# Kernel optimization log

Hardware: AMD Instinct MI355X
Metric: run time of the kernel (lower is better)

The kernel has to match this reference:

```python
import jax, jax.numpy as jnp
from jax import lax
import numpy as np

COMMITMENT = 0.25

def conv(x, w, b, stride, pad):
    # x: NCHW, w: OIHW
    y = lax.conv_general_dilated(x, w, (stride, stride), [(pad, pad), (pad, pad)],
                                 dimension_numbers=('NCHW', 'OIHW', 'NCHW'))
    return y + b[None, :, None, None]

def up2(x):
    # PyTorch nn.Upsample(scale_factor=2, mode='bilinear', align_corners=False)
    b, c, h, w = x.shape
    return jax.image.resize(x, (b, c, 2 * h, 2 * w), method='bilinear')

def vq(z, emb):
    # z: (B, D, H, W); emb: (K, D)
    zc = jnp.transpose(z, (0, 2, 3, 1))          # b h w d
    sh = zc.shape
    flat = zc.reshape(-1, sh[-1])                # (N, D)
    dist = (jnp.sum(flat ** 2, axis=1, keepdims=True)
            + jnp.sum(emb ** 2, axis=1)
            - 2.0 * flat @ emb.T)                # (N, K)
    idx = jnp.argmin(dist, axis=1)               # (N,)
    q = emb[idx].reshape(sh)                     # gather == one-hot @ emb
    e_loss = (lax.stop_gradient(q) - zc) ** 2
    q_loss = (q - lax.stop_gradient(zc)) ** 2
    loss = q_loss + COMMITMENT * e_loss          # (b, h, w, d)
    q_st = zc + lax.stop_gradient(q - zc)        # straight-through
    return jnp.transpose(q_st, (0, 3, 1, 2)), loss

def setup_inputs() -> dict:
    key = jax.random.key(0)
    ks = jax.random.split(key, 32)
    S, K, D, IC = 64, 1024, 64, 3
    def w(k, shape, scale=0.05):
        return jax.random.normal(k, shape, jnp.float32) * scale
    z = lambda n: jnp.zeros((n,), jnp.float32)
    return {
        'x': jax.random.normal(ks[0], (8, IC, 256, 256), jnp.float32),
        'ew1': w(ks[1], (S, IC, 3, 3)),        'eb1': z(S),
        'ew2': w(ks[2], (2 * S, S, 3, 3)),     'eb2': z(2 * S),
        'ew3': w(ks[3], (4 * S, 2 * S, 3, 3)), 'eb3': z(4 * S),
        'ew4': w(ks[4], (8 * S, 4 * S, 3, 3)), 'eb4': z(8 * S),
        'pqw': w(ks[5], (D, 8 * S, 1, 1)),     'pqb': z(D),
        'emb': jax.random.uniform(ks[6], (K, D), jnp.float32, -1.0 / K, 1.0 / K),
        'poqw': w(ks[7], (8 * S, D, 1, 1)),    'poqb': z(8 * S),
        'dw1': w(ks[8], (8 * S, 8 * S, 3, 3)), 'db1': z(8 * S),
        'dw2': w(ks[9], (4 * S, 8 * S, 3, 3)), 'db2': z(4 * S),
        'dw3': w(ks[10], (2 * S, 4 * S, 3, 3)),'db3': z(2 * S),
        'dw4': w(ks[11], (S, 2 * S, 3, 3)),    'db4': z(S),
        'ow': w(ks[12], (IC, S, 3, 3)),        'ob': z(IC),
    }

def reference(x, ew1, eb1, ew2, eb2, ew3, eb3, ew4, eb4, pqw, pqb, emb,
              poqw, poqb, dw1, db1, dw2, db2, dw3, db3, dw4, db4, ow, ob):
    silu = jax.nn.silu
    h = silu(conv(x, ew1, eb1, 1, 1))
    h = silu(conv(h, ew2, eb2, 2, 1))
    h = silu(conv(h, ew3, eb3, 2, 1))
    h = conv(h, ew4, eb4, 2, 1)
    zq = conv(h, pqw, pqb, 1, 0)
    q, loss = vq(zq, emb)
    d = conv(q, poqw, poqb, 1, 0)
    d = up2(silu(conv(d, dw1, db1, 1, 1)))
    d = up2(silu(conv(d, dw2, db2, 1, 1)))
    d = up2(silu(conv(d, dw3, db3, 1, 1)))
    d = conv(d, dw4, db4, 1, 1)
    out = jax.nn.sigmoid(conv(d, ow, ob, 1, 1))
    return out, loss
```

## Files before the change

### kernel.cpp

```cpp
#include <hip/hip_runtime.h>
#include <hip/hip_bf16.h>
#include <math.h>

typedef __hip_bfloat16 bf16;
typedef __attribute__((ext_vector_type(8))) short short8;
typedef __attribute__((ext_vector_type(4))) float f32x4;

static __device__ __forceinline__ float bf2f(unsigned short u) {
  return __uint_as_float(((unsigned int)u) << 16);
}
static __device__ __forceinline__ unsigned short f2bf_bits(float f) {
  unsigned int x = __float_as_uint(f);
  x += 0x7fffu + ((x >> 16) & 1u);
  return (unsigned short)(x >> 16);
}
static __device__ __forceinline__ void sto_bf(bf16* p, float v) {
  *reinterpret_cast<unsigned short*>(p) = f2bf_bits(v);
}
struct F4 { float a, b, c, d; };
static __device__ __forceinline__ F4 ld4bf(const bf16* p) {
  uint2 u = *reinterpret_cast<const uint2*>(p);
  return { bf2f((unsigned short)(u.x & 0xffffu)), bf2f((unsigned short)(u.x >> 16)),
           bf2f((unsigned short)(u.y & 0xffffu)), bf2f((unsigned short)(u.y >> 16)) };
}

static __device__ __forceinline__ void g2l16(const void* g, void* l) {
  __builtin_amdgcn_global_load_lds(
      (const __attribute__((address_space(1))) unsigned int*)g,
      (__attribute__((address_space(3))) unsigned int*)l, 16, 0, 0);
}

__global__ __launch_bounds__(256) void wx_toc(const float* __restrict__ src,
                                              bf16* __restrict__ hi, bf16* __restrict__ lo,
                                              int OC, int IC, int T) {
  int total = T * OC * IC;
  int i = blockIdx.x * 256 + threadIdx.x;
  if (i >= total) return;
  int tap = i / (OC * IC); int r = i - tap * OC * IC;
  int oc = r / IC; int ic = r - oc * IC;
  float v = src[(oc * IC + ic) * T + tap];
  float h = bf2f(f2bf_bits(v));
  sto_bf(hi + i, h);
  if (lo) sto_bf(lo + i, v - h);
}
__global__ __launch_bounds__(256) void wx_tico(const float* __restrict__ src,
                                               float* __restrict__ dst,
                                               int OC, int IC, int T) {
  int total = T * OC * IC;
  int i = blockIdx.x * 256 + threadIdx.x;
  if (i >= total) return;
  int tap = i / (IC * OC); int r = i - tap * IC * OC;
  int ic = r / OC; int oc = r - ic * OC;
  dst[i] = src[(oc * IC + ic) * T + tap];
}

__global__ __launch_bounds__(256) void bzero_knl(bf16* __restrict__ buf, int N, int Hp, int Wp, int C) {
  long per = 2 * Wp + 2 * Hp - 4;
  long total = (long)N * per * C;
  long t = (long)blockIdx.x * 256 + threadIdx.x;
  if (t >= total) return;
  int c = (int)(t % C); long q = t / C;
  int pos = (int)(q % per); int n = (int)(q / per);
  int y, x;
  if (pos < Wp) { y = 0; x = pos; }
  else if (pos < 2 * Wp) { y = Hp - 1; x = pos - Wp; }
  else { int r = pos - 2 * Wp; y = 1 + (r >> 1); x = (r & 1) ? Wp - 1 : 0; }
  *reinterpret_cast<unsigned short*>(&buf[(((long)n * Hp + y) * Wp + x) * C + c]) = 0;
}

template <bool SPLIT, int BM, bool TAP9>
__global__ __launch_bounds__(256) void conv_mfma(
    const bf16* __restrict__ inhi, const bf16* __restrict__ inlo,
    int IHp, int IWp, int IC, int kcLog, int stride,
    const bf16* __restrict__ whi, const bf16* __restrict__ wlo,
    const float* __restrict__ bias, int OC, int OH, int OW,
    int omode, int opad, int OHp, int OWp, int silu,
    void* __restrict__ outp, bf16* __restrict__ outlo)
{
  constexpr int NB = SPLIT ? 2 : 1;
  constexpr int AIW = BM / 32;
  constexpr int MREP = 2;
  constexpr int NREP = (BM == 128) ? 4 : 2;
  __shared__ uint4 ldsA[2][NB][BM * 8];
  __shared__ uint4 ldsB[2][NB][64 * 8];

  const int tid = threadIdx.x;
  const int lane = tid & 63;
  const int wv = tid >> 6;
  const int pixBase = blockIdx.x * BM;
  const int ocBase = blockIdx.y * 64;
  const int OHW = OH * OW;

  int aoff[AIW], asl[AIW];
#pragma unroll
  for (int j = 0; j < AIW; ++j) {
    int I = wv * AIW + j;
    int m = I * 8 + (lane >> 3);
    int icoff = ((lane & 7) ^ (m & 7)) * 8;
    int p = pixBase + m;
    int n = p / OHW; int r = p - n * OHW;
    int oy = r / OW; int ox = r - oy * OW;
    aoff[j] = ((n * IHp + oy * stride) * IWp + ox * stride) * IC + icoff;
    asl[j] = I * 64 + lane;
  }
  int boff[2], bsl[2];
#pragma unroll
  for (int j = 0; j < 2; ++j) {
    int I = wv * 2 + j;
    int ocr = I * 8 + (lane >> 3);
    int icoff = ((lane & 7) ^ (ocr & 7)) * 8;
    boff[j] = (ocBase + ocr) * IC + icoff;
    bsl[j] = I * 64 + lane;
  }

  const int kcMask = (1 << kcLog) - 1;
  const int steps = (TAP9 ? 9 : 1) << kcLog;

  auto stage = [&](int buf, int s) {
    int tap = s >> kcLog;
    int k0 = (s & kcMask) << 6;
    int ta = 0;
    if (TAP9) { int ky = tap / 3, kx = tap - ky * 3; ta = (ky * IWp + kx) * IC; }
    int ga = ta + k0;
#pragma unroll
    for (int j = 0; j < AIW; ++j) {
      g2l16(inhi + aoff[j] + ga, &ldsA[buf][0][asl[j]]);
      if constexpr (SPLIT) g2l16(inlo + aoff[j] + ga, &ldsA[buf][1][asl[j]]);
    }
    int gb = tap * OC * IC + k0;
#pragma unroll
    for (int j = 0; j < 2; ++j) {
      g2l16(whi + boff[j] + gb, &ldsB[buf][0][bsl[j]]);
      if constexpr (SPLIT) g2l16(wlo + boff[j] + gb, &ldsB[buf][1][bsl[j]]);
    }
  };

  const int wrow = (BM == 128) ? wv * 32 : (wv >> 1) * 32;
  const int wcol = (BM == 128) ? 0 : (wv & 1) * 32;

  f32x4 acc[MREP][NREP];
#pragma unroll
  for (int i = 0; i < MREP; ++i)
#pragma unroll
    for (int j = 0; j < NREP; ++j) { acc[i][j][0] = 0.f; acc[i][j][1] = 0.f; acc[i][j][2] = 0.f; acc[i][j][3] = 0.f; }

  stage(0, 0);
  __syncthreads();
  int cur = 0;
  for (int s = 0; s < steps; ++s) {
    if (s + 1 < steps) stage(cur ^ 1, s + 1);
#pragma unroll
    for (int kk = 0; kk < 2; ++kk) {
      int kb = kk * 4 + (lane >> 4);
      short8 af[NB][MREP], bfr[NB][NREP];
#pragma unroll
      for (int mr = 0; mr < MREP; ++mr) {
        int row = wrow + mr * 16 + (lane & 15);
        int slot = row * 8 + (kb ^ (row & 7));
        af[0][mr] = *(const short8*)&ldsA[cur][0][slot];
        if constexpr (SPLIT) af[1][mr] = *(const short8*)&ldsA[cur][1][slot];
      }
#pragma unroll
      for (int nr = 0; nr < NREP; ++nr) {
        int ocr = wcol + nr * 16 + (lane & 15);
        int slot = ocr * 8 + (kb ^ (ocr & 7));
        bfr[0][nr] = *(const short8*)&ldsB[cur][0][slot];
        if constexpr (SPLIT) bfr[1][nr] = *(const short8*)&ldsB[cur][1][slot];
      }
#pragma unroll
      for (int mr = 0; mr < MREP; ++mr)
#pragma unroll
        for (int nr = 0; nr < NREP; ++nr) {
          acc[mr][nr] = __builtin_amdgcn_mfma_f32_16x16x32_bf16(af[0][mr], bfr[0][nr], acc[mr][nr], 0, 0, 0);
          if constexpr (SPLIT) {
            acc[mr][nr] = __builtin_amdgcn_mfma_f32_16x16x32_bf16(af[1][mr], bfr[0][nr], acc[mr][nr], 0, 0, 0);
            acc[mr][nr] = __builtin_amdgcn_mfma_f32_16x16x32_bf16(af[0][mr], bfr[1][nr], acc[mr][nr], 0, 0, 0);
          }
        }
    }
    __syncthreads();
    cur ^= 1;
  }

#pragma unroll
  for (int mr = 0; mr < MREP; ++mr) {
#pragma unroll
    for (int nr = 0; nr < NREP; ++nr) {
      int col = ocBase + wcol + nr * 16 + (lane & 15);
      float bv = bias[col];
#pragma unroll
      for (int r = 0; r < 4; ++r) {
        int row = wrow + mr * 16 + (lane >> 4) * 4 + r;
        float v = acc[mr][nr][r] + bv;
        if (silu) v = v / (1.f + expf(-v));
        int p = pixBase + row;
        if (omode == 0) {
          ((float*)outp)[p * OC + col] = v;
        } else {
          int n = p / OHW; int rr = p - n * OHW;
          int oy = rr / OW; int ox = rr - oy * OW;
          int ob = ((n * OHp + oy + opad) * OWp + ox + opad) * OC + col;
          float h = bf2f(f2bf_bits(v));
          sto_bf((bf16*)outp + ob, h);
          if (omode == 2) sto_bf(outlo + ob, v - h);
        }
      }
    }
  }
}

__global__ __launch_bounds__(256) void e1_knl(const float* __restrict__ x,
                                              const float* __restrict__ w,
                                              const float* __restrict__ bias,
                                              bf16* __restrict__ ahi, bf16* __restrict__ alo) {
  int gw = (blockIdx.x << 2) | (threadIdx.x >> 6);
  int lane = threadIdx.x & 63;
  int ox0 = (gw & 63) << 2;
  int oy = (gw >> 6) & 255;
  int n = gw >> 14;

  float wr[27];
#pragma unroll
  for (int j = 0; j < 27; ++j) wr[j] = w[j * 64 + lane];

  float bv = bias[lane];
  float acc[4] = {bv, bv, bv, bv};

#pragma unroll
  for (int ky = 0; ky < 3; ++ky) {
    int iy = oy - 1 + ky;
    if ((unsigned)iy < 256u) {
#pragma unroll
      for (int ic = 0; ic < 3; ++ic) {
        const float* xr = x + ((n * 3 + ic) * 256 + iy) * 256;
        float xv[6];
#pragma unroll
        for (int j = 0; j < 6; ++j) {
          int ix = ox0 - 1 + j;
          xv[j] = ((unsigned)ix < 256u) ? xr[ix] : 0.f;
        }
#pragma unroll
        for (int kx = 0; kx < 3; ++kx) {
          float wv = wr[(ky * 3 + kx) * 3 + ic];
#pragma unroll
          for (int p = 0; p < 4; ++p) acc[p] = fmaf(xv[p + kx], wv, acc[p]);
        }
      }
    }
  }
#pragma unroll
  for (int p = 0; p < 4; ++p) {
    float v = acc[p] / (1.f + __expf(-acc[p]));
    long ob = (((long)n * 258 + oy + 1) * 258 + (ox0 + p + 1)) * 64 + lane;
    float h = bf2f(f2bf_bits(v));
    sto_bf(ahi + ob, h);
    sto_bf(alo + ob, v - h);
  }
}

__global__ __launch_bounds__(256) void up2_knl(const bf16* __restrict__ in, bf16* __restrict__ out,
                                               int N, int H, int W, int C) {
  int C4 = C >> 2;
  int OW = 2 * W, OH = 2 * H;
  long total = (long)N * OH * OW * C4;
  long tid = (long)blockIdx.x * 256 + threadIdx.x;
  if (tid >= total) return;
  int c4 = (int)(tid % C4); long t = tid / C4;
  int ox = (int)(t % OW); t /= OW;
  int oy = (int)(t % OH); int n = (int)(t / OH);
  float sy = 0.5f * oy - 0.25f, sx = 0.5f * ox - 0.25f;
  int y0 = (int)floorf(sy); float fy = sy - (float)y0;
  int x0 = (int)floorf(sx); float fx = sx - (float)x0;
  int y0c = y0 < 0 ? 0 : y0; int y1c = (y0 + 1 > H - 1) ? (H - 1) : (y0 + 1);
  int x0c = x0 < 0 ? 0 : x0; int x1c = (x0 + 1 > W - 1) ? (W - 1) : (x0 + 1);
  const bf16* base = in + (long)n * H * W * C + c4 * 4;
  F4 t00 = ld4bf(base + ((long)y0c * W + x0c) * C);
  F4 t01 = ld4bf(base + ((long)y0c * W + x1c) * C);
  F4 t10 = ld4bf(base + ((long)y1c * W + x0c) * C);
  F4 t11 = ld4bf(base + ((long)y1c * W + x1c) * C);
  float w00 = (1.f - fy) * (1.f - fx), w01 = (1.f - fy) * fx;
  float w10 = fy * (1.f - fx), w11 = fy * fx;
  union { unsigned short us[4]; uint2 u; } pk;
  pk.us[0] = f2bf_bits(w00 * t00.a + w01 * t01.a + w10 * t10.a + w11 * t11.a);
  pk.us[1] = f2bf_bits(w00 * t00.b + w01 * t01.b + w10 * t10.b + w11 * t11.b);
  pk.us[2] = f2bf_bits(w00 * t00.c + w01 * t01.c + w10 * t10.c + w11 * t11.c);
  pk.us[3] = f2bf_bits(w00 * t00.d + w01 * t01.d + w10 * t10.d + w11 * t11.d);
  *reinterpret_cast<uint2*>(out + (((long)n * (OH + 2) + oy + 1) * (OW + 2) + ox + 1) * C + c4 * 4) = pk.u;
}

__global__ __launch_bounds__(256) void zsplit_knl(const float* __restrict__ src,
                                                  bf16* __restrict__ hi, bf16* __restrict__ lo, int n) {
  int i = blockIdx.x * 256 + threadIdx.x;
  if (i >= n) return;
  float v = src[i];
  float h = bf2f(f2bf_bits(v));
  sto_bf(hi + i, h);
  sto_bf(lo + i, v - h);
}
__global__ __launch_bounds__(256) void nbias_knl(const float* __restrict__ emb, float* __restrict__ nb) {
  int k = blockIdx.x * 256 + threadIdx.x;
  if (k >= 1024) return;
  float s = 0.f;
#pragma unroll
  for (int d = 0; d < 64; ++d) { float e = emb[k * 64 + d]; s = fmaf(e, e, s); }
  nb[k] = -0.5f * s;
}
__global__ __launch_bounds__(256) void vq2_knl(const float* __restrict__ S,
                                               const float* __restrict__ zq,
                                               const float* __restrict__ emb,
                                               bf16* __restrict__ q, float* __restrict__ loss) {
  __shared__ float sd[256];
  __shared__ int si[256];
  int row = blockIdx.x;
  int tid = threadIdx.x;
  const float* Sr = S + (long)row * 1024;
  float best = -3.4e38f; int bi = 0;
#pragma unroll
  for (int j = 0; j < 4; ++j) {
    int k = tid + j * 256;
    float v = Sr[k];
    if (v > best) { best = v; bi = k; }
  }
  sd[tid] = best; si[tid] = bi;
  __syncthreads();
  for (int s = 128; s > 0; s >>= 1) {
    if (tid < s) {
      float od = sd[tid + s]; int oi = si[tid + s];
      if (od > sd[tid] || (od == sd[tid] && oi < si[tid])) { sd[tid] = od; si[tid] = oi; }
    }
    __syncthreads();
  }
  int idx = si[0];
  if (tid < 64) {
    float e = emb[(long)idx * 64 + tid];
    float zv = zq[(long)row * 64 + tid];
    float d = e - zv;
    sto_bf(q + (long)row * 64 + tid, e);
    loss[(long)row * 64 + tid] = 1.25f * d * d;
  }
}

__global__ __launch_bounds__(256) void outc_knl(const bf16* __restrict__ in,
                                                const float* __restrict__ w,
                                                const float* __restrict__ bias,
                                                float* __restrict__ out) {
  int pix = blockIdx.x * 256 + threadIdx.x;
  int x = pix & 255;
  int y = (pix >> 8) & 255;
  int n = pix >> 16;
  float a0 = bias[0], a1 = bias[1], a2 = bias[2];
#pragma unroll
  for (int ky = 0; ky < 3; ++ky) {
#pragma unroll
    for (int kx = 0; kx < 3; ++kx) {
      const bf16* ip = in + (((long)(n * 258 + y + ky)) * 258 + (x + kx)) * 64;
      const int t = ky * 3 + kx;
#pragma unroll
      for (int g = 0; g < 8; ++g) {
        short8 v = *reinterpret_cast<const short8*>(ip + g * 8);
#pragma unroll
        for (int j = 0; j < 8; ++j) {
          float f = bf2f((unsigned short)v[j]);
          int ic = g * 8 + j;
          a0 = fmaf(f, w[(t * 64 + ic) * 3 + 0], a0);
          a1 = fmaf(f, w[(t * 64 + ic) * 3 + 1], a1);
          a2 = fmaf(f, w[(t * 64 + ic) * 3 + 2], a2);
        }
      }
    }
  }
  long ob = ((long)n * 3) * 65536 + ((long)y << 8) + x;
  out[ob]          = 1.f / (1.f + __expf(-a0));
  out[ob + 65536]  = 1.f / (1.f + __expf(-a1));
  out[ob + 131072] = 1.f / (1.f + __expf(-a2));
}

extern "C" void kernel_launch(void* const* d_in, const int* in_sizes, int n_in,
                              void* d_out, int out_size, void* d_ws, size_t ws_size,
                              hipStream_t stream) {
  (void)in_sizes; (void)n_in; (void)out_size; (void)ws_size;
  const float* x    = (const float*)d_in[0];
  const float* ew1  = (const float*)d_in[1];  const float* eb1 = (const float*)d_in[2];
  const float* ew2  = (const float*)d_in[3];  const float* eb2 = (const float*)d_in[4];
  const float* ew3  = (const float*)d_in[5];  const float* eb3 = (const float*)d_in[6];
  const float* ew4  = (const float*)d_in[7];  const float* eb4 = (const float*)d_in[8];
  const float* pqw  = (const float*)d_in[9];  const float* pqb = (const float*)d_in[10];
  const float* emb  = (const float*)d_in[11];
  const float* poqw = (const float*)d_in[12]; const float* poqb = (const float*)d_in[13];
  const float* dw1  = (const float*)d_in[14]; const float* db1 = (const float*)d_in[15];
  const float* dw2  = (const float*)d_in[16]; const float* db2 = (const float*)d_in[17];
  const float* dw3  = (const float*)d_in[18]; const float* db3 = (const float*)d_in[19];
  const float* dw4  = (const float*)d_in[20]; const float* db4 = (const float*)d_in[21];
  const float* oww  = (const float*)d_in[22]; const float* ob  = (const float*)d_in[23];

  char* wsb = (char*)d_ws;
  size_t off = 0;
  auto alloc = [&](size_t b) -> char* {
    char* p = wsb + off;
    off = (off + b + 255) & ~(size_t)255;
    return p;
  };

  float* w_e1   = (float*)alloc(1728 * 4);
  float* w_ow   = (float*)alloc(1728 * 4);
  float* nbias  = (float*)alloc(1024 * 4);
  bf16* w_eh  = (bf16*)alloc(65536 * 2);   bf16* w_el  = (bf16*)alloc(65536 * 2);
  bf16* w_e2h = (bf16*)alloc(73728 * 2);   bf16* w_e2l = (bf16*)alloc(73728 * 2);
  bf16* w_e3h = (bf16*)alloc(294912 * 2);  bf16* w_e3l = (bf16*)alloc(294912 * 2);
  bf16* w_e4h = (bf16*)alloc(1179648 * 2); bf16* w_e4l = (bf16*)alloc(1179648 * 2);
  bf16* w_pqh = (bf16*)alloc(32768 * 2);   bf16* w_pql = (bf16*)alloc(32768 * 2);
  bf16* w_poq = (bf16*)alloc(32768 * 2);
  bf16* w_d1  = (bf16*)alloc(2359296 * 2);
  bf16* w_d2  = (bf16*)alloc(1179648 * 2);
  bf16* w_d3  = (bf16*)alloc(294912 * 2);
  bf16* w_d4  = (bf16*)alloc(73728 * 2);

  char* RA = alloc(68161536);
  char* RB = alloc(68161536);
  char* RC = alloc(28360704);

  bf16* a1h = (bf16*)RA;
  bf16* a1l = (bf16*)(RA + 34080768);
  float* Sbuf = (float*)RA;
  bf16* zqh  = (bf16*)(RA + 33554432);
  bf16* zql  = (bf16*)(RA + 34603008);
  bf16* u3h_ = (bf16*)RA;

  bf16* a2h = (bf16*)RB;
  bf16* a2l = (bf16*)(RB + 17305600);
  bf16* a3h = (bf16*)(RB + 34611200);
  bf16* a3l = (bf16*)(RB + 43532288);
  bf16* a4h = (bf16*)(RB + 52453376);
  bf16* a4l = (bf16*)(RB + 56647680);
  float* zqF = (float*)(RB + 60841984);

  bf16* u2h_ = (bf16*)RB;
  bf16* c4h_ = (bf16*)RB;
  bf16* c3h_ = (bf16*)(RB + 34611200);
  bf16* c2h_ = (bf16*)(RB + 51388416);
  bf16* c1h_ = (bf16*)(RB + 59777024);

  bf16* qb   = (bf16*)RC;
  bf16* poqO = (bf16*)(RC + 1048576);
  bf16* u1h_ = (bf16*)(RC + 10518528);

  float* out0 = (float*)d_out;
  float* loss = out0 + 1572864;

  auto G1 = [](long n) { return dim3((unsigned)((n + 255) / 256)); };

  wx_tico<<<G1(1728), 256, 0, stream>>>(ew1, w_e1, 64, 3, 9);
  wx_tico<<<G1(1728), 256, 0, stream>>>(oww, w_ow, 3, 64, 9);
  nbias_knl<<<4, 256, 0, stream>>>(emb, nbias);
  wx_toc<<<G1(65536), 256, 0, stream>>>(emb, w_eh, w_el, 1024, 64, 1);
  wx_toc<<<G1(73728), 256, 0, stream>>>(ew2, w_e2h, w_e2l, 128, 64, 9);
  wx_toc<<<G1(294912), 256, 0, stream>>>(ew3, w_e3h, w_e3l, 256, 128, 9);
  wx_toc<<<G1(1179648), 256, 0, stream>>>(ew4, w_e4h, w_e4l, 512, 256, 9);
  wx_toc<<<G1(32768), 256, 0, stream>>>(pqw, w_pqh, w_pql, 64, 512, 1);
  wx_toc<<<G1(32768), 256, 0, stream>>>(poqw, w_poq, (bf16*)nullptr, 512, 64, 1);
  wx_toc<<<G1(2359296), 256, 0, stream>>>(dw1, w_d1, (bf16*)nullptr, 512, 512, 9);
  wx_toc<<<G1(1179648), 256, 0, stream>>>(dw2, w_d2, (bf16*)nullptr, 256, 512, 9);
  wx_toc<<<G1(294912), 256, 0, stream>>>(dw3, w_d3, (bf16*)nullptr, 128, 256, 9);
  wx_toc<<<G1(73728), 256, 0, stream>>>(dw4, w_d4, (bf16*)nullptr, 64, 128, 9);

  auto bz = [&](bf16* p, int N, int Hp, int Wp, int C) {
    long tot = (long)N * (2 * Wp + 2 * Hp - 4) * C;
    bzero_knl<<<G1(tot), 256, 0, stream>>>(p, N, Hp, Wp, C);
  };
  bz(a1h, 4, 258, 258, 64); bz(a1l, 4, 258, 258, 64);
  bz(a2h, 4, 130, 130, 128); bz(a2l, 4, 130, 130, 128);
  bz(a3h, 4, 66, 66, 256);   bz(a3l, 4, 66, 66, 256);

  for (int h = 0; h < 2; ++h) {
    const float* xh = x + (size_t)h * 786432;
    e1_knl<<<16384, 256, 0, stream>>>(xh, w_e1, eb1, a1h, a1l);
    conv_mfma<true, 64, true><<<dim3(1024, 2), 256, 0, stream>>>(
        a1h, a1l, 258, 258, 64, 0, 2, w_e2h, w_e2l, eb2, 128, 128, 128, 2, 1, 130, 130, 1, a2h, a2l);
    conv_mfma<true, 64, true><<<dim3(256, 4), 256, 0, stream>>>(
        a2h, a2l, 130, 130, 128, 1, 2, w_e3h, w_e3l, eb3, 256, 64, 64, 2, 1, 66, 66, 1, a3h, a3l);
    conv_mfma<true, 64, true><<<dim3(64, 8), 256, 0, stream>>>(
        a3h, a3l, 66, 66, 256, 2, 2, w_e4h, w_e4l, eb4, 512, 32, 32, 2, 0, 32, 32, 0, a4h, a4l);
    conv_mfma<true, 64, false><<<dim3(64, 1), 256, 0, stream>>>(
        a4h, a4l, 32, 32, 512, 3, 1, w_pqh, w_pql, pqb, 64, 32, 32, 0, 0, 32, 32, 0,
        zqF + (size_t)h * 262144, nullptr);
  }

  zsplit_knl<<<G1(524288), 256, 0, stream>>>(zqF, zqh, zql, 524288);
  conv_mfma<true, 64, false><<<dim3(128, 16), 256, 0, stream>>>(
      zqh, zql, 32, 32, 64, 0, 1, w_eh, w_el, nbias, 1024, 32, 32, 0, 0, 32, 32, 0, Sbuf, nullptr);
  vq2_knl<<<8192, 256, 0, stream>>>(Sbuf, zqF, emb, qb, loss);

  bz(poqO, 8, 34, 34, 512);
  bz(u1h_, 4, 66, 66, 512);
  conv_mfma<false, 128, false><<<dim3(64, 8), 256, 0, stream>>>(
      qb, nullptr, 32, 32, 64, 0, 1, w_poq, nullptr, poqb, 512, 32, 32, 1, 1, 34, 34, 0, poqO, nullptr);

  for (int h = 0; h < 2; ++h) {
    bf16* pin = poqO + (size_t)h * 4 * 34 * 34 * 512;
    float* oout = out0 + (size_t)h * 786432;
    conv_mfma<false, 128, true><<<dim3(32, 8), 256, 0, stream>>>(
        pin, nullptr, 34, 34, 512, 3, 1, w_d1, nullptr, db1, 512, 32, 32, 1, 0, 32, 32, 1, c1h_, nullptr);
    up2_knl<<<G1(4l * 64 * 64 * 128), 256, 0, stream>>>(c1h_, u1h_, 4, 32, 32, 512);
    conv_mfma<false, 128, true><<<dim3(128, 4), 256, 0, stream>>>(
        u1h_, nullptr, 66, 66, 512, 3, 1, w_d2, nullptr, db2, 256, 64, 64, 1, 0, 64, 64, 1, c2h_, nullptr);
    bz(u2h_, 4, 130, 130, 256);
    up2_knl<<<G1(4l * 128 * 128 * 64), 256, 0, stream>>>(c2h_, u2h_, 4, 64, 64, 256);
    conv_mfma<false, 128, true><<<dim3(512, 2), 256, 0, stream>>>(
        u2h_, nullptr, 130, 130, 256, 2, 1, w_d3, nullptr, db3, 128, 128, 128, 1, 0, 128, 128, 1, c3h_, nullptr);
    bz(u3h_, 4, 258, 258, 128);
    up2_knl<<<G1(4l * 256 * 256 * 32), 256, 0, stream>>>(c3h_, u3h_, 4, 128, 128, 128);
    bz(c4h_, 4, 258, 258, 64);
    conv_mfma<false, 128, true><<<dim3(2048, 1), 256, 0, stream>>>(
        u3h_, nullptr, 258, 258, 128, 1, 1, w_d4, nullptr, db4, 64, 256, 256, 1, 1, 258, 258, 0, c4h_, nullptr);
    outc_knl<<<1024, 256, 0, stream>>>(c4h_, w_ow, ob, oout);
  }
}
```

Before: 1.413 ms.

## Triple-buffer LDS staging with partial vmcnt waits for non-split conv

For the non-split bf16 conv path, the shared-memory staging goes from double to triple buffering. Global-to-LDS loads are issued two k-steps ahead, and the full __syncthreads is replaced by s_waitcnt vmcnt(6) plus a raw barrier, so only the older loads must land before each step. The aim is to hide global memory latency behind MFMA compute. In exchange it uses more LDS per block, which can lower occupancy, and the hard-coded vmcnt depends on the exact number of loads issued per stage.

After: 1.544 ms. 1.09x slower.

```diff
diff --git a/kernel.cpp b/kernel.cpp
--- a/kernel.cpp
+++ b/kernel.cpp
@@ -78,11 +78,12 @@
     void* __restrict__ outp, bf16* __restrict__ outlo)
 {
   constexpr int NB = SPLIT ? 2 : 1;
+  constexpr int NBUF = SPLIT ? 2 : 3;
   constexpr int AIW = BM / 32;
   constexpr int MREP = 2;
   constexpr int NREP = (BM == 128) ? 4 : 2;
-  __shared__ uint4 ldsA[2][NB][BM * 8];
-  __shared__ uint4 ldsB[2][NB][64 * 8];
+  __shared__ uint4 ldsA[NBUF][NB][BM * 8];
+  __shared__ uint4 ldsB[NBUF][NB][64 * 8];
 
   const int tid = threadIdx.x;
   const int lane = tid & 63;
@@ -144,11 +145,7 @@
 #pragma unroll
     for (int j = 0; j < NREP; ++j) { acc[i][j][0] = 0.f; acc[i][j][1] = 0.f; acc[i][j][2] = 0.f; acc[i][j][3] = 0.f; }
 
-  stage(0, 0);
-  __syncthreads();
-  int cur = 0;
-  for (int s = 0; s < steps; ++s) {
-    if (s + 1 < steps) stage(cur ^ 1, s + 1);
+  auto compute = [&](int cur) {
 #pragma unroll
     for (int kk = 0; kk < 2; ++kk) {
       int kb = kk * 4 + (lane >> 4);
@@ -178,8 +175,39 @@
           }
         }
     }
+  };
+
+  if constexpr (SPLIT) {
+    stage(0, 0);
     __syncthreads();
-    cur ^= 1;
+    int cur = 0;
+    for (int s = 0; s < steps; ++s) {
+      if (s + 1 < steps) stage(cur ^ 1, s + 1);
+      compute(cur);
+      __syncthreads();
+      cur ^= 1;
+    }
+  } else {
+    stage(0, 0);
+    if (steps > 1) {
+      stage(1, 1);
+      asm volatile("s_waitcnt vmcnt(6)" ::: "memory");
+    } else {
+      asm volatile("s_waitcnt vmcnt(0)" ::: "memory");
+    }
+    __builtin_amdgcn_s_barrier();
+    asm volatile("" ::: "memory");
+    for (int s = 0; s < steps; ++s) {
+      int cur = s % 3;
+      if (s + 2 < steps) stage((s + 2) % 3, s + 2);
+      compute(cur);
+      if (s + 1 < steps) {
+        if (s + 2 < steps) asm volatile("s_waitcnt vmcnt(6)" ::: "memory");
+        else               asm volatile("s_waitcnt vmcnt(0)" ::: "memory");
+        __builtin_amdgcn_s_barrier();
+        asm volatile("" ::: "memory");
+      }
+    }
   }
 
 #pragma unroll
```
